# Kernel optimization log

Measured on AMD Instinct MI355X. Metric: run time of the kernel, lower is better.

## Reference

```python
import jax, jax.numpy as jnp
import numpy as np

SCALING = 2.0  # lora alpha / rank
B, S, H = 4, 2048, 4096
N = 4096  # q/k/v out features
R = 16    # lora rank


def setup_inputs() -> dict:
    key = jax.random.key(0)
    ks = jax.random.split(key, 10)
    std_w = 1.0 / np.sqrt(H)
    inp = {
        'X': jax.random.normal(ks[0], (B, S, H), dtype=jnp.float32),
        'QW': jax.random.normal(ks[1], (N, H), dtype=jnp.float32) * std_w,
        'QA': jax.random.normal(ks[2], (R, H), dtype=jnp.float32) * std_w,
        'QB': jax.random.normal(ks[3], (N, R), dtype=jnp.float32) * 0.01,
        'KW': jax.random.normal(ks[4], (N, H), dtype=jnp.float32) * std_w,
        'KA': jax.random.normal(ks[5], (R, H), dtype=jnp.float32) * std_w,
        'KB': jax.random.normal(ks[6], (N, R), dtype=jnp.float32) * 0.01,
        'VW': jax.random.normal(ks[7], (N, H), dtype=jnp.float32) * std_w,
        'VA': jax.random.normal(ks[8], (R, H), dtype=jnp.float32) * std_w,
        'VB': jax.random.normal(ks[9], (N, R), dtype=jnp.float32) * 0.01,
    }
    return inp


def _matmul_lora(X, W, A, Bm, scaling):
    # Y = X @ W.T + scaling * (X @ A.T) @ B.T ; X: [bs, h], W: [n, h], A: [r, h], B: [n, r]
    base = jnp.einsum('bsh,nh->bsn', X, W)
    lora = jnp.einsum('bsr,nr->bsn', jnp.einsum('bsh,rh->bsr', X, A), Bm)
    return base + scaling * lora


def reference(X, QW, QA, QB, KW, KA, KB, VW, VA, VB):
    Q = _matmul_lora(X, QW, QA, QB, SCALING)
    K = _matmul_lora(X, KW, KA, KB, SCALING)
    V = _matmul_lora(X, VW, VA, VB, SCALING)
    return (Q, K, V)
```

## Files before the change

kernel.cpp:

```cpp
#include <hip/hip_runtime.h>


typedef unsigned short u16;
typedef __attribute__((ext_vector_type(4))) float  f32x4;
typedef __attribute__((ext_vector_type(8))) __bf16 bf16x8;
typedef __attribute__((ext_vector_type(8))) short  s16x8;

#define MDIM 8192
#define NDIM 4096
#define KDIM 4096

__device__ __forceinline__ u16 f2bf(float f) {
    union { float f; unsigned int u; } v;
    v.f = f;
    unsigned int r = v.u + 0x7FFFu + ((v.u >> 16) & 1u);
    return (u16)(r >> 16);
}

__global__ void __launch_bounds__(256) cvt_x_kernel(const float* __restrict__ X,
                                                    u16* __restrict__ Xb, int nvec8) {
    int stride = gridDim.x * blockDim.x;
    for (int i = blockIdx.x * blockDim.x + threadIdx.x; i < nvec8; i += stride) {
        f32x4 x0 = ((const f32x4*)X)[2 * i];
        f32x4 x1 = ((const f32x4*)X)[2 * i + 1];
        s16x8 o;
        o[0] = (short)f2bf(x0[0]); o[1] = (short)f2bf(x0[1]);
        o[2] = (short)f2bf(x0[2]); o[3] = (short)f2bf(x0[3]);
        o[4] = (short)f2bf(x1[0]); o[5] = (short)f2bf(x1[1]);
        o[6] = (short)f2bf(x1[2]); o[7] = (short)f2bf(x1[3]);
        ((s16x8*)Xb)[i] = o;
    }
}

__global__ void __launch_bounds__(256) merge_w3_kernel(const float* __restrict__ QW,
                                                       const float* __restrict__ QA,
                                                       const float* __restrict__ QB,
                                                       const float* __restrict__ KW,
                                                       const float* __restrict__ KA,
                                                       const float* __restrict__ KB,
                                                       const float* __restrict__ VW,
                                                       const float* __restrict__ VA,
                                                       const float* __restrict__ VB,
                                                       u16* __restrict__ WbAll) {
    const int z = blockIdx.z;
    const float* W  = (z == 0) ? QW : (z == 1) ? KW : VW;
    const float* A  = (z == 0) ? QA : (z == 1) ? KA : VA;
    const float* Bm = (z == 0) ? QB : (z == 1) ? KB : VB;
    u16* Wb = WbAll + (size_t)z * NDIM * KDIM;

    __shared__ float As[16][64];
    const int t  = threadIdx.x;
    const int hb = blockIdx.x * 64;
    const int nb = blockIdx.y * 128;

    {
        int r = t >> 4, c = (t & 15) * 4;
        *(f32x4*)&As[r][c] = *(const f32x4*)&A[r * 4096 + hb + c];
    }
    __syncthreads();

    const int hl = (t & 7) * 8;
    const int n0 = nb + (t >> 3) * 4;

    float bv[4][16];
    float s[4][8];
#pragma unroll
    for (int i = 0; i < 4; i++) {
        const float* br = &Bm[(size_t)(n0 + i) * 16];
#pragma unroll
        for (int r = 0; r < 16; r++) bv[i][r] = 2.0f * br[r];
        f32x4 w0 = *(const f32x4*)&W[(size_t)(n0 + i) * 4096 + hb + hl];
        f32x4 w1 = *(const f32x4*)&W[(size_t)(n0 + i) * 4096 + hb + hl + 4];
        s[i][0] = w0[0]; s[i][1] = w0[1]; s[i][2] = w0[2]; s[i][3] = w0[3];
        s[i][4] = w1[0]; s[i][5] = w1[1]; s[i][6] = w1[2]; s[i][7] = w1[3];
    }
#pragma unroll
    for (int r = 0; r < 16; r++) {
        f32x4 a0 = *(const f32x4*)&As[r][hl];
        f32x4 a1 = *(const f32x4*)&As[r][hl + 4];
#pragma unroll
        for (int i = 0; i < 4; i++) {
            s[i][0] += bv[i][r] * a0[0]; s[i][1] += bv[i][r] * a0[1];
            s[i][2] += bv[i][r] * a0[2]; s[i][3] += bv[i][r] * a0[3];
            s[i][4] += bv[i][r] * a1[0]; s[i][5] += bv[i][r] * a1[1];
            s[i][6] += bv[i][r] * a1[2]; s[i][7] += bv[i][r] * a1[3];
        }
    }
#pragma unroll
    for (int i = 0; i < 4; i++) {
        s16x8 o;
#pragma unroll
        for (int j = 0; j < 8; j++) o[j] = (short)f2bf(s[i][j]);
        *(s16x8*)&Wb[(size_t)(n0 + i) * 4096 + hb + hl] = o;
    }
}


#define BM 256
#define BN 256
#define BK 64

#define BAR() asm volatile("s_barrier" ::: "memory")
#define WAIT_VM(n) asm volatile("s_waitcnt vmcnt(" #n ")" ::: "memory")
#define PRIO(p) __builtin_amdgcn_s_setprio(p)

__global__ void __launch_bounds__(512, 2) gemm8_kernel(const u16* __restrict__ Xb,
                                                       const u16* __restrict__ Wb,
                                                       float* __restrict__ out) {
    extern __shared__ char lds[];

    const int t    = threadIdx.x;
    const int lane = t & 63;
    const int w    = t >> 6;
    const int wr   = w >> 2;
    const int wn   = w & 3;
    const int lr   = lane & 15;
    const int lkq  = lane >> 4;
    const int lr7  = lr & 7;

    const int orig = blockIdx.x;
    const int z    = orig >> 9;
    const int r0   = orig & 511;
    const int i_   = (r0 & 7) * 64 + (r0 >> 3);
    const int nT = i_ & 15;
    const int mT = i_ >> 4;
    const int mBase = mT * BM;
    const int nBase = nT * BN;

    const u16* Wp = Wb + (size_t)z * NDIM * KDIM;
    const char* gA = (const char*)Xb + (size_t)mBase * (KDIM * 2);
    const char* gB = (const char*)Wp + (size_t)nBase * (KDIM * 2);

    char* ldsA0 = lds;
    char* ldsA1 = lds + 32768;
    char* ldsB0 = lds + 65536;
    char* ldsB1 = lds + 98304;

    const int blkrow = lane >> 3;
    const int colswz = ((lane & 7) ^ blkrow) << 4;
    const size_t stg0 = (size_t)(((w << 1) | 0) * 8 + blkrow) * (KDIM * 2) + colswz;
    const size_t stg1 = (size_t)(((w << 1) | 1) * 8 + blkrow) * (KDIM * 2) + colswz;
    const int ldsStg0 = (((w << 1) | 0) << 10) + lane * 16;
    const int ldsStg1 = (((w << 1) | 1) << 10) + lane * 16;

#define STAGE(ldsTile, gtile, h, kt)                                              \
  { __builtin_amdgcn_global_load_lds(                                             \
        (const __attribute__((address_space(1))) void*)((gtile) + stg0 +          \
            (size_t)(h) * (128 * KDIM * 2) + (size_t)(kt) * 128),                 \
        (__attribute__((address_space(3))) void*)((ldsTile) + (h) * 16384 + ldsStg0), \
        16, 0, 0);                                                                \
    __builtin_amdgcn_global_load_lds(                                             \
        (const __attribute__((address_space(1))) void*)((gtile) + stg1 +          \
            (size_t)(h) * (128 * KDIM * 2) + (size_t)(kt) * 128),                 \
        (__attribute__((address_space(3))) void*)((ldsTile) + (h) * 16384 + ldsStg1), \
        16, 0, 0); }

    const int csA = (lkq << 4) ^ (lr7 << 4);
    const int rA0 = (wr * 128 + lr) * 128;
    const int rB0 = (wn * 64 + lr) * 128;
#define RD_A(tile, mi, kk) (*(const bf16x8*)((tile) + rA0 + (mi) * 2048 + (((kk) << 6) ^ csA)))
#define RD_B(tile, ni, kk) (*(const bf16x8*)((tile) + rB0 + (ni) * 2048 + (((kk) << 6) ^ csA)))

    f32x4 acc[8][4] = {};
    bf16x8 aR1[4][2], aR2[4][2], bR[4][2];

#define MFMA_Q(AF, mbase, nbase)                                                   \
    PRIO(1);                                                                       \
    _Pragma("unroll") for (int mi = 0; mi < 4; ++mi)                               \
    _Pragma("unroll") for (int ni = 0; ni < 2; ++ni)                               \
    _Pragma("unroll") for (int kk = 0; kk < 2; ++kk)                               \
      acc[(mbase) + mi][(nbase) + ni] = __builtin_amdgcn_mfma_f32_16x16x32_bf16(   \
          AF[mi][kk], bR[(nbase) + ni][kk], acc[(mbase) + mi][(nbase) + ni], 0, 0, 0); \
    PRIO(0);

#define PH1(pA, pB, STG)                                                           \
  { BAR();                                                                         \
    aR1[0][0] = RD_A(pA, 0, 0); aR1[0][1] = RD_A(pA, 0, 1);                        \
    bR[0][0]  = RD_B(pB, 0, 0); bR[0][1]  = RD_B(pB, 0, 1);                        \
    aR1[1][0] = RD_A(pA, 1, 0); aR1[1][1] = RD_A(pA, 1, 1);                        \
    bR[1][0]  = RD_B(pB, 1, 0); bR[1][1]  = RD_B(pB, 1, 1);                        \
    aR1[2][0] = RD_A(pA, 2, 0); aR1[2][1] = RD_A(pA, 2, 1);                        \
    aR1[3][0] = RD_A(pA, 3, 0); aR1[3][1] = RD_A(pA, 3, 1);                        \
    STG; MFMA_Q(aR1, 0, 0) }

#define PH2(pA, pB, STG)                                                           \
  { BAR();                                                                         \
    bR[2][0] = RD_B(pB, 2, 0); bR[2][1] = RD_B(pB, 2, 1);                          \
    bR[3][0] = RD_B(pB, 3, 0); bR[3][1] = RD_B(pB, 3, 1);                          \
    aR2[0][0] = RD_A(pA, 4, 0); aR2[0][1] = RD_A(pA, 4, 1);                        \
    aR2[1][0] = RD_A(pA, 5, 0); aR2[1][1] = RD_A(pA, 5, 1);                        \
    STG; MFMA_Q(aR1, 0, 2) }

#define PH3(pA, STG)                                                               \
  { BAR();                                                                         \
    aR2[2][0] = RD_A(pA, 6, 0); aR2[2][1] = RD_A(pA, 6, 1);                        \
    aR2[3][0] = RD_A(pA, 7, 0); aR2[3][1] = RD_A(pA, 7, 1);                        \
    STG; MFMA_Q(aR2, 4, 0) }

#define PH4(STG, VMW)                                                              \
  { BAR(); STG; VMW; MFMA_Q(aR2, 4, 2) }

#define PH4F()                                                                     \
  { BAR(); MFMA_Q(aR2, 4, 2) }

    STAGE(ldsA0, gA, 0, 0); STAGE(ldsA0, gA, 1, 0);
    STAGE(ldsB0, gB, 0, 0); STAGE(ldsB0, gB, 1, 0);
    STAGE(ldsB1, gB, 0, 1); STAGE(ldsB1, gB, 1, 1);
    STAGE(ldsA1, gA, 0, 1);
    WAIT_VM(6);

    for (int i = 0; i < 31; ++i) {
        const int T = 2 * i;
        PH1(ldsA0, ldsB0, STAGE(ldsA1, gA, 1, T + 1));
        PH2(ldsA0, ldsB0, );
        PH3(ldsA0,        STAGE(ldsB0, gB, 0, T + 2));
        PH4(              STAGE(ldsB0, gB, 1, T + 2), WAIT_VM(4));
        PH1(ldsA1, ldsB1, STAGE(ldsA0, gA, 0, T + 2));
        PH2(ldsA1, ldsB1, STAGE(ldsA0, gA, 1, T + 2));
        PH3(ldsA1,        STAGE(ldsB1, gB, 0, T + 3));
        PH4(              { STAGE(ldsB1, gB, 1, T + 3)
                            STAGE(ldsA1, gA, 0, T + 3) }, WAIT_VM(6));
    }

    PH1(ldsA0, ldsB0, STAGE(ldsA1, gA, 1, 63));
    PH2(ldsA0, ldsB0, );
    PH3(ldsA0, );
    PH4(, WAIT_VM(0));
    PH1(ldsA1, ldsB1, );
    PH2(ldsA1, ldsB1, );
    PH3(ldsA1, );
    PH4F();

    float* C = out + (size_t)z * MDIM * NDIM;
#pragma unroll
    for (int mi = 0; mi < 8; ++mi) {
#pragma unroll
        for (int ni = 0; ni < 4; ++ni) {
            const int col  = nBase + wn * 64 + ni * 16 + lr;
            const int row0 = mBase + wr * 128 + mi * 16 + lkq * 4;
            f32x4 v = acc[mi][ni];
#pragma unroll
            for (int j = 0; j < 4; ++j)
                C[(size_t)(row0 + j) * NDIM + col] = v[j];
        }
    }
}

extern "C" void kernel_launch(void* const* d_in, const int* in_sizes, int n_in,
                              void* d_out, int out_size, void* d_ws, size_t ws_size,
                              hipStream_t stream) {
    const float* X  = (const float*)d_in[0];
    const float* QW = (const float*)d_in[1];
    const float* QA = (const float*)d_in[2];
    const float* QB = (const float*)d_in[3];
    const float* KW = (const float*)d_in[4];
    const float* KA = (const float*)d_in[5];
    const float* KB = (const float*)d_in[6];
    const float* VW = (const float*)d_in[7];
    const float* VA = (const float*)d_in[8];
    const float* VB = (const float*)d_in[9];
    float* out = (float*)d_out;

    u16* Xb = (u16*)d_ws;
    u16* Wb = (u16*)((char*)d_ws + (size_t)MDIM * KDIM * 2);

    (void)hipFuncSetAttribute((const void*)gemm8_kernel,
                              hipFuncAttributeMaxDynamicSharedMemorySize, 131072);

    cvt_x_kernel<<<2048, 256, 0, stream>>>(X, Xb, (MDIM * KDIM) / 8);

    dim3 wgrid(4096 / 64, 4096 / 128, 3);
    merge_w3_kernel<<<wgrid, 256, 0, stream>>>(QW, QA, QB, KW, KA, KB, VW, VA, VB, Wb);

    gemm8_kernel<<<dim3(16 * 32 * 3), dim3(512), 131072, stream>>>(Xb, Wb, out);
}
```

Measured before the change: 773.0 us.

## Restructure GEMM main loop from four phases to two per K-tile

Merges the four barrier-separated phases per K-tile into two. Each phase now issues two global-to-LDS stages up front, then does its LDS reads and two MFMA quadrants, so there are half as many barriers per tile. The prologue and wait counts are adjusted, and the A tile for T+1 is now staged inside the first phase. This cuts synchronization overhead, but it also changes the interleaving of memory and compute and raises register pressure.

Result: no change. 779.4 us (+0.8%).

```diff
diff --git a/kernel.cpp b/kernel.cpp
--- a/kernel.cpp
+++ b/kernel.cpp
@@ -173,63 +173,45 @@
           AF[mi][kk], bR[(nbase) + ni][kk], acc[(mbase) + mi][(nbase) + ni], 0, 0, 0); \
     PRIO(0);
 
-#define PH1(pA, pB, STG)                                                           \
-  { BAR();                                                                         \
+#define PHA(pA, pB, STG1, STG2)                                                    \
+  { BAR(); STG1; STG2;                                                             \
     aR1[0][0] = RD_A(pA, 0, 0); aR1[0][1] = RD_A(pA, 0, 1);                        \
     bR[0][0]  = RD_B(pB, 0, 0); bR[0][1]  = RD_B(pB, 0, 1);                        \
     aR1[1][0] = RD_A(pA, 1, 0); aR1[1][1] = RD_A(pA, 1, 1);                        \
     bR[1][0]  = RD_B(pB, 1, 0); bR[1][1]  = RD_B(pB, 1, 1);                        \
     aR1[2][0] = RD_A(pA, 2, 0); aR1[2][1] = RD_A(pA, 2, 1);                        \
     aR1[3][0] = RD_A(pA, 3, 0); aR1[3][1] = RD_A(pA, 3, 1);                        \
-    STG; MFMA_Q(aR1, 0, 0) }
-
-#define PH2(pA, pB, STG)                                                           \
-  { BAR();                                                                         \
-    bR[2][0] = RD_B(pB, 2, 0); bR[2][1] = RD_B(pB, 2, 1);                          \
-    bR[3][0] = RD_B(pB, 3, 0); bR[3][1] = RD_B(pB, 3, 1);                          \
+    bR[2][0]  = RD_B(pB, 2, 0); bR[2][1]  = RD_B(pB, 2, 1);                        \
+    bR[3][0]  = RD_B(pB, 3, 0); bR[3][1]  = RD_B(pB, 3, 1);                        \
     aR2[0][0] = RD_A(pA, 4, 0); aR2[0][1] = RD_A(pA, 4, 1);                        \
     aR2[1][0] = RD_A(pA, 5, 0); aR2[1][1] = RD_A(pA, 5, 1);                        \
-    STG; MFMA_Q(aR1, 0, 2) }
-
-#define PH3(pA, STG)                                                               \
-  { BAR();                                                                         \
+    MFMA_Q(aR1, 0, 0) MFMA_Q(aR1, 0, 2) }
+
+#define PHB(pA, STG1, STG2, VMW)                                                   \
+  { BAR(); STG1; STG2;                                                             \
     aR2[2][0] = RD_A(pA, 6, 0); aR2[2][1] = RD_A(pA, 6, 1);                        \
     aR2[3][0] = RD_A(pA, 7, 0); aR2[3][1] = RD_A(pA, 7, 1);                        \
-    STG; MFMA_Q(aR2, 4, 0) }
-
-#define PH4(STG, VMW)                                                              \
-  { BAR(); STG; VMW; MFMA_Q(aR2, 4, 2) }
-
-#define PH4F()                                                                     \
-  { BAR(); MFMA_Q(aR2, 4, 2) }
+    MFMA_Q(aR2, 4, 0) MFMA_Q(aR2, 4, 2) VMW; }
 
     STAGE(ldsA0, gA, 0, 0); STAGE(ldsA0, gA, 1, 0);
     STAGE(ldsB0, gB, 0, 0); STAGE(ldsB0, gB, 1, 0);
     STAGE(ldsB1, gB, 0, 1); STAGE(ldsB1, gB, 1, 1);
-    STAGE(ldsA1, gA, 0, 1);
-    WAIT_VM(6);
+    WAIT_VM(4);
 
     for (int i = 0; i < 31; ++i) {
         const int T = 2 * i;
-        PH1(ldsA0, ldsB0, STAGE(ldsA1, gA, 1, T + 1));
-        PH2(ldsA0, ldsB0, );
-        PH3(ldsA0,        STAGE(ldsB0, gB, 0, T + 2));
-        PH4(              STAGE(ldsB0, gB, 1, T + 2), WAIT_VM(4));
-        PH1(ldsA1, ldsB1, STAGE(ldsA0, gA, 0, T + 2));
-        PH2(ldsA1, ldsB1, STAGE(ldsA0, gA, 1, T + 2));
-        PH3(ldsA1,        STAGE(ldsB1, gB, 0, T + 3));
-        PH4(              { STAGE(ldsB1, gB, 1, T + 3)
-                            STAGE(ldsA1, gA, 0, T + 3) }, WAIT_VM(6));
-    }
-
-    PH1(ldsA0, ldsB0, STAGE(ldsA1, gA, 1, 63));
-    PH2(ldsA0, ldsB0, );
-    PH3(ldsA0, );
-    PH4(, WAIT_VM(0));
-    PH1(ldsA1, ldsB1, );
-    PH2(ldsA1, ldsB1, );
-    PH3(ldsA1, );
-    PH4F();
+        PHA(ldsA0, ldsB0, STAGE(ldsA1, gA, 0, T + 1), STAGE(ldsA1, gA, 1, T + 1));
+        PHB(ldsA0,        STAGE(ldsB0, gB, 0, T + 2), STAGE(ldsB0, gB, 1, T + 2),
+            WAIT_VM(4));
+        PHA(ldsA1, ldsB1, STAGE(ldsA0, gA, 0, T + 2), STAGE(ldsA0, gA, 1, T + 2));
+        PHB(ldsA1,        STAGE(ldsB1, gB, 0, T + 3), STAGE(ldsB1, gB, 1, T + 3),
+            WAIT_VM(4));
+    }
+
+    PHA(ldsA0, ldsB0, STAGE(ldsA1, gA, 0, 63), STAGE(ldsA1, gA, 1, 63));
+    PHB(ldsA0, , , WAIT_VM(0));
+    PHA(ldsA1, ldsB1, , );
+    PHB(ldsA1, , , );
 
     float* C = out + (size_t)z * MDIM * NDIM;
 #pragma unroll
```
